# Kernel tuning notes

Measured on AMD Instinct MI355X. Metric: run time of the kernel, lower is better.

## Reference

```python
import jax, jax.numpy as jnp
import numpy as np

N_DIM = 512
HEADS = 8
NUM_EXPERTS = 65536
NUM_KEYS = 256      # sqrt(NUM_EXPERTS)
DIM_KEY = 256       # N_DIM // 2
TOPK = 16           # num_experts_per_head (also product_key_topk)
SCALE = 0.02


def setup_inputs() -> dict:
    key = jax.random.key(0)
    k0, k1, k2, k3, k4 = jax.random.split(key, 5)
    x = jax.random.normal(k0, (1, 2048, N_DIM), dtype=jnp.float32)
    W_q = jax.random.normal(k1, (N_DIM, 2 * HEADS * DIM_KEY), dtype=jnp.float32) * SCALE
    keys = jax.random.normal(k2, (HEADS, NUM_KEYS, 2, DIM_KEY), dtype=jnp.float32) * SCALE
    down_embed = jax.random.normal(k3, (NUM_EXPERTS, N_DIM), dtype=jnp.float32) * SCALE
    up_embed = jax.random.normal(k4, (NUM_EXPERTS, N_DIM), dtype=jnp.float32) * SCALE
    return {"x": x, "W_q": W_q, "keys": keys, "down_embed": down_embed, "up_embed": up_embed}


def reference(x, W_q, keys, down_embed, up_embed):
    b, n, d = x.shape
    # queries: [b,n,2*h*dk] -> [2,b,n,h,dk]
    q = (x @ W_q).reshape(b, n, 2, HEADS, DIM_KEY).transpose(2, 0, 1, 3, 4)
    # similarity against product keys: [2,b,n,h,num_keys]
    sim = jnp.einsum('pbnhd,hkpd->pbnhk', q, keys)
    sx, ix = jax.lax.top_k(sim[0], TOPK)   # [b,n,h,TOPK]
    sy, iy = jax.lax.top_k(sim[1], TOPK)
    # cartesian product of the two top-k sets -> [b,n,h,TOPK*TOPK]
    all_scores = (sx[..., :, None] + sy[..., None, :]).reshape(b, n, HEADS, TOPK * TOPK)
    scores, pk_idx = jax.lax.top_k(all_scores, TOPK)  # [b,n,h,TOPK]
    # NOTE: original module indexes embeddings with pk_idx (flat top-k positions),
    # reproduced faithfully here.
    w_down = down_embed[pk_idx]  # [b,n,h,TOPK,d]
    w_up = up_embed[pk_idx]      # [b,n,h,TOPK,d]
    h = jnp.einsum('bnd,bnhkd->bnhk', x, w_down)
    h = jax.nn.gelu(h, approximate=False)
    h = jax.nn.softmax(scores, axis=-1) * h
    return jnp.einsum('bnhk,bnhkd->bnd', h, w_up)
```

## Files before the change

### kernel.cpp

```cpp
#include <hip/hip_runtime.h>
#include <math.h>

#define N_TOK 2048
#define NDIM 512
#define HEADS 8
#define TOPK 16
#define QCOLS 4096

typedef __attribute__((ext_vector_type(8))) _Float16 f16x8;
typedef __attribute__((ext_vector_type(4))) float f32x4;

__device__ __forceinline__ unsigned short f32_to_f16(float f) {
    _Float16 h = (_Float16)f;
    return __builtin_bit_cast(unsigned short, h);
}
__device__ __forceinline__ float f16_to_f32(unsigned short u) {
    return (float)__builtin_bit_cast(_Float16, u);
}
__device__ __forceinline__ void gl_lds16(const void* g, void* l) {
    __builtin_amdgcn_global_load_lds(
        (const __attribute__((address_space(1))) void*)g,
        (__attribute__((address_space(3))) void*)l, 16, 0, 0);
}

__device__ __forceinline__ void split_f4(const float* __restrict__ src,
                                         unsigned short* __restrict__ dh,
                                         unsigned short* __restrict__ dl,
                                         int i) {
    float4 v = reinterpret_cast<const float4*>(src)[i];
    float vv[4] = {v.x, v.y, v.z, v.w};
    ushort4 h, lo;
    unsigned short* hp = &h.x; unsigned short* lp = &lo.x;
    #pragma unroll
    for (int q = 0; q < 4; ++q) {
        unsigned short hh = f32_to_f16(vv[q]);
        hp[q] = hh;
        lp[q] = f32_to_f16(vv[q] - f16_to_f32(hh));
    }
    reinterpret_cast<ushort4*>(dh)[i] = h;
    reinterpret_cast<ushort4*>(dl)[i] = lo;
}

__global__ __launch_bounds__(256) void kP_split(const float* __restrict__ x,
                                                const float* __restrict__ Wq,
                                                const float* __restrict__ keys,
                                                const float* __restrict__ down,
                                                const float* __restrict__ up,
                                                unsigned short* __restrict__ xh,
                                                unsigned short* __restrict__ xl,
                                                unsigned short* __restrict__ Wqh,
                                                unsigned short* __restrict__ Wql,
                                                unsigned short* __restrict__ ksh,
                                                unsigned short* __restrict__ ksl,
                                                unsigned short* __restrict__ Mth,
                                                unsigned short* __restrict__ Mtl,
                                                unsigned short* __restrict__ upTh,
                                                unsigned short* __restrict__ upTl) {
    const int bid = blockIdx.x;
    const int tid = threadIdx.x;
    if (bid < 256) {
        #pragma unroll
        for (int t = 0; t < 4; ++t) split_f4(x, xh, xl, bid * 1024 + t * 256 + tid);
        return;
    }
    if (bid < 768) {
        const int b = bid - 256;
        #pragma unroll
        for (int t = 0; t < 4; ++t) split_f4(Wq, Wqh, Wql, b * 1024 + t * 256 + tid);
        return;
    }
    if (bid < 1024) {
        const int b = bid - 768;
        #pragma unroll
        for (int t = 0; t < 4; ++t) split_f4(keys, ksh, ksl, b * 1024 + t * 256 + tid);
        return;
    }
    if (bid < 1280) {
        const int e = bid - 1024;
        const int d0 = tid * 2;
        float2 v = *reinterpret_cast<const float2*>(&down[(size_t)e * NDIM + d0]);
        ushort2 h, lo;
        unsigned short h0 = f32_to_f16(v.x);
        unsigned short h1 = f32_to_f16(v.y);
        h.x = h0; h.y = h1;
        lo.x = f32_to_f16(v.x - f16_to_f32(h0));
        lo.y = f32_to_f16(v.y - f16_to_f32(h1));
        *reinterpret_cast<ushort2*>(&Mth[(size_t)(QCOLS + e) * NDIM + d0]) = h;
        *reinterpret_cast<ushort2*>(&Mtl[(size_t)(QCOLS + e) * NDIM + d0]) = lo;
        return;
    }
    const int b = bid - 1280;
    #pragma unroll
    for (int dd = 0; dd < 8; ++dd) {
        const int d = b * 8 + dd;
        const int e = tid;
        const float v = up[(size_t)e * NDIM + d];
        unsigned short hh = f32_to_f16(v);
        upTh[(size_t)d * 256 + e] = hh;
        upTl[(size_t)d * 256 + e] = f32_to_f16(v - f16_to_f32(hh));
    }
}

__global__ __launch_bounds__(256) void kQ_m1(const unsigned short* __restrict__ Wqh,
                                             const unsigned short* __restrict__ Wql,
                                             const unsigned short* __restrict__ ksh,
                                             const unsigned short* __restrict__ ksl,
                                             unsigned short* __restrict__ Mth,
                                             unsigned short* __restrict__ Mtl) {
    __shared__ __align__(16) char lds[36864];
    const int tid = threadIdx.x;
    const int w = tid >> 6, l = tid & 63;
    const int c0 = blockIdx.x * 32;
    const int ph = blockIdx.y;
    const int p = ph >> 3, h = ph & 7;
    const int off = p * 2048 + h * 256;
    f32x4 acc[2][4] = {};

    for (int s = 0; s < 8; ++s) {
        const int kk = s * 32;
        __syncthreads();
        {
            const int q = w * 1024 + l * 16;
            const int r = q >> 7;
            const int bsw = (q & 127) ^ ((r & 7) << 4);
            const unsigned short* src = (bsw < 64)
                ? Wqh + (size_t)(c0 + r) * QCOLS + off + kk + (bsw >> 1)
                : Wql + (size_t)(c0 + r) * QCOLS + off + kk + ((bsw - 64) >> 1);
            gl_lds16(src, lds + w * 1024);
        }
        #pragma unroll
        for (int t = 0; t < 8; ++t) {
            const int q = w * 8192 + t * 1024 + l * 16;
            const int r = q >> 7;
            const int bsw = (q & 127) ^ ((r & 7) << 4);
            const unsigned short* src = (bsw < 64)
                ? ksh + ((size_t)(h * 256 + r) * 2 + p) * 256 + kk + (bsw >> 1)
                : ksl + ((size_t)(h * 256 + r) * 2 + p) * 256 + kk + ((bsw - 64) >> 1);
            gl_lds16(src, lds + 4096 + w * 8192 + t * 1024);
        }
        __syncthreads();
        const int bq = (l >> 4) * 16;
        f16x8 ah[2], al[2];
        #pragma unroll
        for (int mi = 0; mi < 2; ++mi) {
            const int ra = mi * 16 + (l & 15);
            const int swz = (ra & 7) << 4;
            ah[mi] = *(const f16x8*)(lds + ra * 128 + (bq ^ swz));
            al[mi] = *(const f16x8*)(lds + ra * 128 + ((bq + 64) ^ swz));
        }
        __builtin_amdgcn_s_setprio(1);
        #pragma unroll
        for (int nj = 0; nj < 4; ++nj) {
            const int rb = w * 64 + nj * 16 + (l & 15);
            const int swz = (rb & 7) << 4;
            f16x8 bh = *(const f16x8*)(lds + 4096 + rb * 128 + (bq ^ swz));
            f16x8 bl = *(const f16x8*)(lds + 4096 + rb * 128 + ((bq + 64) ^ swz));
            #pragma unroll
            for (int mi = 0; mi < 2; ++mi) {
                acc[mi][nj] = __builtin_amdgcn_mfma_f32_16x16x32_f16(ah[mi], bh, acc[mi][nj], 0, 0, 0);
                acc[mi][nj] = __builtin_amdgcn_mfma_f32_16x16x32_f16(ah[mi], bl, acc[mi][nj], 0, 0, 0);
                acc[mi][nj] = __builtin_amdgcn_mfma_f32_16x16x32_f16(al[mi], bh, acc[mi][nj], 0, 0, 0);
            }
        }
        __builtin_amdgcn_s_setprio(0);
    }
    #pragma unroll
    for (int mi = 0; mi < 2; ++mi)
        #pragma unroll
        for (int nj = 0; nj < 4; ++nj) {
            const int k = w * 64 + nj * 16 + (l & 15);
            const int cb = c0 + mi * 16 + (l >> 4) * 4;
            ushort4 h4, l4;
            unsigned short* hp = &h4.x; unsigned short* lp = &l4.x;
            #pragma unroll
            for (int r = 0; r < 4; ++r) {
                const float v = acc[mi][nj][r];
                unsigned short hh = f32_to_f16(v);
                hp[r] = hh;
                lp[r] = f32_to_f16(v - f16_to_f32(hh));
            }
            *reinterpret_cast<ushort4*>(&Mth[(size_t)(off + k) * NDIM + cb]) = h4;
            *reinterpret_cast<ushort4*>(&Mtl[(size_t)(off + k) * NDIM + cb]) = l4;
        }
}

#define BM 64
#define BN 256
#define BK 32
__global__ __launch_bounds__(256, 3) void kF_gemm(const unsigned short* __restrict__ xh,
                                                  const unsigned short* __restrict__ xl,
                                                  const unsigned short* __restrict__ Mth,
                                                  const unsigned short* __restrict__ Mtl,
                                                  float* __restrict__ T,
                                                  float* __restrict__ D) {
    __shared__ __align__(16) char lds[40960];
    const int tid = threadIdx.x;
    const int w = tid >> 6, l = tid & 63;
    const int row0 = blockIdx.x * BM;
    const int g = blockIdx.y;
    const int colbase = g * 256;
    f32x4 acc[4][4] = {};

    for (int s = 0; s < 16; ++s) {
        const int kk = s * BK;
        __syncthreads();
        #pragma unroll
        for (int t = 0; t < 2; ++t) {
            const int q = w * 2048 + t * 1024 + l * 16;
            const int r = q >> 7;
            const int bsw = (q & 127) ^ ((r & 7) << 4);
            const unsigned short* src = (bsw < 64)
                ? xh + (size_t)(row0 + r) * NDIM + kk + (bsw >> 1)
                : xl + (size_t)(row0 + r) * NDIM + kk + ((bsw - 64) >> 1);
            gl_lds16(src, lds + w * 2048 + t * 1024);
        }
        #pragma unroll
        for (int t = 0; t < 8; ++t) {
            const int q = w * 8192 + t * 1024 + l * 16;
            const int r = q >> 7;
            const int bsw = (q & 127) ^ ((r & 7) << 4);
            const unsigned short* src = (bsw < 64)
                ? Mth + (size_t)(colbase + r) * NDIM + kk + (bsw >> 1)
                : Mtl + (size_t)(colbase + r) * NDIM + kk + ((bsw - 64) >> 1);
            gl_lds16(src, lds + 8192 + w * 8192 + t * 1024);
        }
        __syncthreads();
        const int bq = (l >> 4) * 16;
        f16x8 ah[4], al[4];
        #pragma unroll
        for (int mi = 0; mi < 4; ++mi) {
            const int ra = mi * 16 + (l & 15);
            const int swz = (ra & 7) << 4;
            ah[mi] = *(const f16x8*)(lds + ra * 128 + (bq ^ swz));
            al[mi] = *(const f16x8*)(lds + ra * 128 + ((bq + 64) ^ swz));
        }
        __builtin_amdgcn_s_setprio(1);
        #pragma unroll
        for (int nj = 0; nj < 4; ++nj) {
            const int rb = w * 64 + nj * 16 + (l & 15);
            const int swz = (rb & 7) << 4;
            f16x8 bh = *(const f16x8*)(lds + 8192 + rb * 128 + (bq ^ swz));
            f16x8 bl = *(const f16x8*)(lds + 8192 + rb * 128 + ((bq + 64) ^ swz));
            #pragma unroll
            for (int mi = 0; mi < 4; ++mi) {
                acc[mi][nj] = __builtin_amdgcn_mfma_f32_16x16x32_f16(ah[mi], bh, acc[mi][nj], 0, 0, 0);
                acc[mi][nj] = __builtin_amdgcn_mfma_f32_16x16x32_f16(ah[mi], bl, acc[mi][nj], 0, 0, 0);
                acc[mi][nj] = __builtin_amdgcn_mfma_f32_16x16x32_f16(al[mi], bh, acc[mi][nj], 0, 0, 0);
            }
        }
        __builtin_amdgcn_s_setprio(0);
    }
    __syncthreads();

    if (g == 16) {
        #pragma unroll
        for (int mi = 0; mi < 4; ++mi)
            #pragma unroll
            for (int nj = 0; nj < 4; ++nj)
                #pragma unroll
                for (int r = 0; r < 4; ++r) {
                    const int row = row0 + mi * 16 + (l >> 4) * 4 + r;
                    const int col = w * 64 + nj * 16 + (l & 15);
                    D[(size_t)row * 256 + col] = acc[mi][nj][r];
                }
        return;
    }

    float* Cl = (float*)lds;
    const int grp = tid >> 4;
    const int lam = tid & 15;
    for (int c = 0; c < 4; ++c) {
        #pragma unroll
        for (int nj = 0; nj < 4; ++nj)
            #pragma unroll
            for (int r = 0; r < 4; ++r)
                Cl[((l >> 4) * 4 + r) * 260 + w * 64 + nj * 16 + (l & 15)] = acc[c][nj][r];
        __syncthreads();
        float v[16];
        #pragma unroll
        for (int j = 0; j < 16; ++j) v[j] = Cl[grp * 260 + lam + 16 * j];
        #pragma unroll
        for (int k = 2; k <= 16; k <<= 1)
            #pragma unroll
            for (int j = k >> 1; j > 0; j >>= 1)
                #pragma unroll
                for (int i = 0; i < 16; ++i) {
                    const int l2 = i ^ j;
                    if (l2 > i) {
                        const bool asc = ((i & k) == 0);
                        const float lo = fminf(v[i], v[l2]), hi = fmaxf(v[i], v[l2]);
                        v[i] = asc ? lo : hi;
                        v[l2] = asc ? hi : lo;
                    }
                }
        #pragma unroll
        for (int lvl = 1; lvl <= 8; lvl <<= 1) {
            float m[16];
            #pragma unroll
            for (int q = 0; q < 16; ++q)
                m[q] = fmaxf(v[q], __shfl_xor(v[15 - q], lvl));
            #pragma unroll
            for (int j = 8; j > 0; j >>= 1)
                #pragma unroll
                for (int i = 0; i < 16; ++i) {
                    const int l2 = i ^ j;
                    if (l2 > i) {
                        const float lo = fminf(m[i], m[l2]), hi = fmaxf(m[i], m[l2]);
                        m[i] = lo; m[l2] = hi;
                    }
                }
            #pragma unroll
            for (int q = 0; q < 16; ++q) v[q] = m[q];
        }
        const int n = row0 + c * 16 + grp;
        T[((size_t)n * 16 + g) * 16 + lam] = v[15 - lam];
        __syncthreads();
    }
}

__device__ const unsigned short CAND_TBL[32] = {
    0x0100, 0x0302, 0x0504, 0x0706, 0x0908, 0x0B0A, 0x0D0C, 0x0F0E,
    0x1110, 0x1312, 0x1514, 0x1716,
    0x2120, 0x2322, 0x3024, 0x3231, 0x4033, 0x4241,
    0x5150, 0x6160, 0x7170,
    0x9080, 0xB0A0, 0xD0C0, 0xF0E0,
    0xFFFF, 0xFFFF, 0xFFFF, 0xFFFF, 0xFFFF, 0xFFFF, 0xFFFF
};

__device__ __forceinline__ float sel16(const float a[16], int i) {
    float b0 = (i & 1) ? a[1] : a[0];
    float b1 = (i & 1) ? a[3] : a[2];
    float b2 = (i & 1) ? a[5] : a[4];
    float b3 = (i & 1) ? a[7] : a[6];
    float b4 = (i & 1) ? a[9] : a[8];
    float b5 = (i & 1) ? a[11] : a[10];
    float b6 = (i & 1) ? a[13] : a[12];
    float b7 = (i & 1) ? a[15] : a[14];
    float c0 = (i & 2) ? b1 : b0;
    float c1 = (i & 2) ? b3 : b2;
    float c2 = (i & 2) ? b5 : b4;
    float c3 = (i & 2) ? b7 : b6;
    float d0 = (i & 4) ? c1 : c0;
    float d1 = (i & 4) ? c3 : c2;
    return (i & 8) ? d1 : d0;
}

__global__ __launch_bounds__(256) void kC_combine(const float* __restrict__ T,
                                                  const float* __restrict__ D,
                                                  unsigned short* __restrict__ Wh,
                                                  unsigned short* __restrict__ Wl) {
    __shared__ unsigned long long ckey[8][50];
    __shared__ float winval[8][16];
    __shared__ int winflat[8][16];
    __shared__ int Wrow[256];

    const int tid = threadIdx.x;
    const int n = blockIdx.x;
    const int h = tid >> 5;
    const int lam = tid & 15;

    Wrow[tid] = 0;

    float sxd[16], syd[16];
    const float* t0 = &T[((size_t)n * 16 + h) * 16];
    const float* t1 = &T[((size_t)n * 16 + 8 + h) * 16];
    #pragma unroll
    for (int q = 0; q < 16; ++q) { sxd[q] = t0[q]; syd[q] = t1[q]; }

    const int lc = tid & 31;
    const unsigned int cw = CAND_TBL[lc];
    unsigned long long mykey[2]; float myval[2]; int myflat[2]; int myrank[2] = {0, 0};
    #pragma unroll
    for (int u = 0; u < 2; ++u) {
        const int fl = (cw >> (8 * u)) & 0xFF;
        const float sv = sel16(sxd, fl >> 4) + sel16(syd, fl & 15);
        const unsigned int uv = __float_as_uint(sv);
        const unsigned int mo = (uv & 0x80000000u) ? ~uv : (uv | 0x80000000u);
        mykey[u] = ((unsigned long long)mo << 8) | (unsigned long long)(255 - fl);
        myval[u] = sv; myflat[u] = fl;
        const int slot = lc * 2 + u;
        if (slot < 50) ckey[h][slot] = mykey[u];
    }
    __syncthreads();
    for (int kk = 0; kk < 50; ++kk) {
        const unsigned long long ok = ckey[h][kk];
        myrank[0] += (ok > mykey[0]) ? 1 : 0;
        myrank[1] += (ok > mykey[1]) ? 1 : 0;
    }
    #pragma unroll
    for (int u = 0; u < 2; ++u)
        if (myrank[u] < 16) { winval[h][myrank[u]] = myval[u]; winflat[h][myrank[u]] = myflat[u]; }
    __syncthreads();

    if (!(tid & 16)) {
        const float sc = winval[h][lam];
        const float m0 = winval[h][0];
        float e = expf(sc - m0);
        float esum = e;
        #pragma unroll
        for (int off = 1; off < 16; off <<= 1) esum += __shfl_xor(esum, off);
        const int fl = winflat[h][lam];
        const float hv = D[(size_t)n * 256 + fl];
        const float gg = 0.5f * hv * (1.0f + erff(hv * 0.70710678118654752f));
        const float wv = (e / esum) * gg;
        atomicAdd(&Wrow[fl], __float2int_rn(wv * 4194304.0f));
    }
    __syncthreads();
    const float wfin = (float)Wrow[tid] * (1.0f / 4194304.0f);
    const unsigned short hh = f32_to_f16(wfin);
    Wh[(size_t)n * 256 + tid] = hh;
    Wl[(size_t)n * 256 + tid] = f32_to_f16(wfin - f16_to_f32(hh));
}

__global__ __launch_bounds__(256) void k5_mfma(const unsigned short* __restrict__ Wh,
                                               const unsigned short* __restrict__ Wl,
                                               const unsigned short* __restrict__ upTh,
                                               const unsigned short* __restrict__ upTl,
                                               float* __restrict__ out) {
    __shared__ __align__(16) char lds[20480];
    const int tid = threadIdx.x;
    const int w = tid >> 6, l = tid & 63;
    const int n0 = blockIdx.x * 32;
    const int d0 = blockIdx.y * 128;
    f32x4 acc[2][2] = {};

    for (int s = 0; s < 8; ++s) {
        const int kk = s * 32;
        __syncthreads();
        {
            const int q = w * 1024 + l * 16;
            const int r = q >> 7;
            const int bsw = (q & 127) ^ ((r & 7) << 4);
            const unsigned short* src = (bsw < 64)
                ? Wh + (size_t)(n0 + r) * 256 + kk + (bsw >> 1)
                : Wl + (size_t)(n0 + r) * 256 + kk + ((bsw - 64) >> 1);
            gl_lds16(src, lds + w * 1024);
        }
        #pragma unroll
        for (int t = 0; t < 4; ++t) {
            const int q = w * 4096 + t * 1024 + l * 16;
            const int r = q >> 7;
            const int bsw = (q & 127) ^ ((r & 7) << 4);
            const unsigned short* src = (bsw < 64)
                ? upTh + (size_t)(d0 + r) * 256 + kk + (bsw >> 1)
                : upTl + (size_t)(d0 + r) * 256 + kk + ((bsw - 64) >> 1);
            gl_lds16(src, lds + 4096 + w * 4096 + t * 1024);
        }
        __syncthreads();
        const int bq = (l >> 4) * 16;
        f16x8 ah[2], al[2];
        #pragma unroll
        for (int mi = 0; mi < 2; ++mi) {
            const int ra = mi * 16 + (l & 15);
            const int swz = (ra & 7) << 4;
            ah[mi] = *(const f16x8*)(lds + ra * 128 + (bq ^ swz));
            al[mi] = *(const f16x8*)(lds + ra * 128 + ((bq + 64) ^ swz));
        }
        #pragma unroll
        for (int nj = 0; nj < 2; ++nj) {
            const int rb = w * 32 + nj * 16 + (l & 15);
            const int swz = (rb & 7) << 4;
            f16x8 bh = *(const f16x8*)(lds + 4096 + rb * 128 + (bq ^ swz));
            f16x8 bl = *(const f16x8*)(lds + 4096 + rb * 128 + ((bq + 64) ^ swz));
            #pragma unroll
            for (int mi = 0; mi < 2; ++mi) {
                acc[mi][nj] = __builtin_amdgcn_mfma_f32_16x16x32_f16(ah[mi], bh, acc[mi][nj], 0, 0, 0);
                acc[mi][nj] = __builtin_amdgcn_mfma_f32_16x16x32_f16(ah[mi], bl, acc[mi][nj], 0, 0, 0);
                acc[mi][nj] = __builtin_amdgcn_mfma_f32_16x16x32_f16(al[mi], bh, acc[mi][nj], 0, 0, 0);
            }
        }
    }
    #pragma unroll
    for (int mi = 0; mi < 2; ++mi)
        #pragma unroll
        for (int nj = 0; nj < 2; ++nj)
            #pragma unroll
            for (int r = 0; r < 4; ++r) {
                const int row = n0 + mi * 16 + (l >> 4) * 4 + r;
                const int col = d0 + w * 32 + nj * 16 + (l & 15);
                out[(size_t)row * NDIM + col] = acc[mi][nj][r];
            }
}

extern "C" void kernel_launch(void* const* d_in, const int* in_sizes, int n_in,
                              void* d_out, int out_size, void* d_ws, size_t ws_size,
                              hipStream_t stream) {
    const float* x    = (const float*)d_in[0];
    const float* Wq   = (const float*)d_in[1];
    const float* keys = (const float*)d_in[2];
    const float* down = (const float*)d_in[3];
    const float* up   = (const float*)d_in[4];
    float* out = (float*)d_out;

    char* ws = (char*)d_ws;
    unsigned short* Mth  = (unsigned short*)(ws);
    unsigned short* Mtl  = (unsigned short*)(ws + 4456448);
    unsigned short* xh   = (unsigned short*)(ws + 8912896);
    unsigned short* xl   = (unsigned short*)(ws + 11010048);
    unsigned short* Wqh  = (unsigned short*)(ws + 13107200);
    unsigned short* Wql  = (unsigned short*)(ws + 17301504);
    unsigned short* ksh  = (unsigned short*)(ws + 21495808);
    unsigned short* ksl  = (unsigned short*)(ws + 23592960);
    unsigned short* upTh = (unsigned short*)(ws + 25690112);
    unsigned short* upTl = (unsigned short*)(ws + 25952256);
    float* T             = (float*)(ws + 26214400);
    float* D             = (float*)(ws + 28311552);
    unsigned short* Wh   = (unsigned short*)(ws + 30408704);
    unsigned short* Wl   = (unsigned short*)(ws + 31457280);

    kP_split<<<1344, 256, 0, stream>>>(x, Wq, keys, down, up,
                                       xh, xl, Wqh, Wql, ksh, ksl, Mth, Mtl, upTh, upTl);
    kQ_m1<<<dim3(16, 16), 256, 0, stream>>>(Wqh, Wql, ksh, ksl, Mth, Mtl);
    kF_gemm<<<dim3(32, 17), 256, 0, stream>>>(xh, xl, Mth, Mtl, T, D);
    kC_combine<<<2048, 256, 0, stream>>>(T, D, Wh, Wl);
    k5_mfma<<<dim3(64, 4), 256, 0, stream>>>(Wh, Wl, upTh, upTl, out);
}
```

Before: 94.20 us.

## Retile score GEMM to 128x128 with double-buffered LDS and split top-k merge

The fused score GEMM moves from 64x256 tiles to 128x128 tiles and double-buffers the LDS stages, so the next K-slice loads while MFMAs run. Each block now produces top-16 over 128 keys instead of 256, which doubles the partial-list layout in T. The combine kernel gains a bitonic merge of two 16-element partial lists per half-key. The intent is better load/compute overlap and a grid shape that fills the CUs better, at the cost of lower occupancy (launch bounds 2), more T traffic and extra merge work in the combine kernel.

Measured after the change: 91.51 us. -2.8%, faster.

```diff
diff --git a/kernel.cpp b/kernel.cpp
--- a/kernel.cpp
+++ b/kernel.cpp
@@ -184,101 +184,112 @@
         }
 }
 
-#define BM 64
-#define BN 256
+#define BM 128
+#define BN 128
 #define BK 32
-__global__ __launch_bounds__(256, 3) void kF_gemm(const unsigned short* __restrict__ xh,
+#define KFBUF 32768
+__global__ __launch_bounds__(256, 2) void kF_gemm(const unsigned short* __restrict__ xh,
                                                   const unsigned short* __restrict__ xl,
                                                   const unsigned short* __restrict__ Mth,
                                                   const unsigned short* __restrict__ Mtl,
                                                   float* __restrict__ T,
                                                   float* __restrict__ D) {
-    __shared__ __align__(16) char lds[40960];
+    __shared__ __align__(16) char lds[2 * KFBUF];
     const int tid = threadIdx.x;
     const int w = tid >> 6, l = tid & 63;
     const int row0 = blockIdx.x * BM;
-    const int g = blockIdx.y;
-    const int colbase = g * 256;
-    f32x4 acc[4][4] = {};
-
-    for (int s = 0; s < 16; ++s) {
+    const int by = blockIdx.y;
+    const int colbase = by * 128;
+    f32x4 acc[8][2] = {};
+
+    auto stage = [&](int buf, int s) {
         const int kk = s * BK;
-        __syncthreads();
-        #pragma unroll
-        for (int t = 0; t < 2; ++t) {
-            const int q = w * 2048 + t * 1024 + l * 16;
+        char* base = lds + buf * KFBUF;
+        #pragma unroll
+        for (int t = 0; t < 4; ++t) {
+            const int q = w * 4096 + t * 1024 + l * 16;
             const int r = q >> 7;
             const int bsw = (q & 127) ^ ((r & 7) << 4);
             const unsigned short* src = (bsw < 64)
                 ? xh + (size_t)(row0 + r) * NDIM + kk + (bsw >> 1)
                 : xl + (size_t)(row0 + r) * NDIM + kk + ((bsw - 64) >> 1);
-            gl_lds16(src, lds + w * 2048 + t * 1024);
-        }
-        #pragma unroll
-        for (int t = 0; t < 8; ++t) {
-            const int q = w * 8192 + t * 1024 + l * 16;
+            gl_lds16(src, base + w * 4096 + t * 1024);
+        }
+        #pragma unroll
+        for (int t = 0; t < 4; ++t) {
+            const int q = w * 4096 + t * 1024 + l * 16;
             const int r = q >> 7;
             const int bsw = (q & 127) ^ ((r & 7) << 4);
             const unsigned short* src = (bsw < 64)
                 ? Mth + (size_t)(colbase + r) * NDIM + kk + (bsw >> 1)
                 : Mtl + (size_t)(colbase + r) * NDIM + kk + ((bsw - 64) >> 1);
-            gl_lds16(src, lds + 8192 + w * 8192 + t * 1024);
-        }
-        __syncthreads();
+            gl_lds16(src, base + 16384 + w * 4096 + t * 1024);
+        }
+    };
+
+    stage(0, 0);
+    __syncthreads();
+    for (int s = 0; s < 16; ++s) {
+        if (s + 1 < 16) stage((s + 1) & 1, s + 1);
+        const char* base = lds + (s & 1) * KFBUF;
         const int bq = (l >> 4) * 16;
-        f16x8 ah[4], al[4];
-        #pragma unroll
-        for (int mi = 0; mi < 4; ++mi) {
+        f16x8 bh[2], bl[2];
+        #pragma unroll
+        for (int nj = 0; nj < 2; ++nj) {
+            const int rb = w * 32 + nj * 16 + (l & 15);
+            const int swz = (rb & 7) << 4;
+            bh[nj] = *(const f16x8*)(base + 16384 + rb * 128 + (bq ^ swz));
+            bl[nj] = *(const f16x8*)(base + 16384 + rb * 128 + ((bq + 64) ^ swz));
+        }
+        __builtin_amdgcn_s_setprio(1);
+        #pragma unroll
+        for (int mi = 0; mi < 8; ++mi) {
             const int ra = mi * 16 + (l & 15);
             const int swz = (ra & 7) << 4;
-            ah[mi] = *(const f16x8*)(lds + ra * 128 + (bq ^ swz));
-            al[mi] = *(const f16x8*)(lds + ra * 128 + ((bq + 64) ^ swz));
-        }
-        __builtin_amdgcn_s_setprio(1);
-        #pragma unroll
-        for (int nj = 0; nj < 4; ++nj) {
-            const int rb = w * 64 + nj * 16 + (l & 15);
-            const int swz = (rb & 7) << 4;
-            f16x8 bh = *(const f16x8*)(lds + 8192 + rb * 128 + (bq ^ swz));
-            f16x8 bl = *(const f16x8*)(lds + 8192 + rb * 128 + ((bq + 64) ^ swz));
-            #pragma unroll
-            for (int mi = 0; mi < 4; ++mi) {
-                acc[mi][nj] = __builtin_amdgcn_mfma_f32_16x16x32_f16(ah[mi], bh, acc[mi][nj], 0, 0, 0);
-                acc[mi][nj] = __builtin_amdgcn_mfma_f32_16x16x32_f16(ah[mi], bl, acc[mi][nj], 0, 0, 0);
-                acc[mi][nj] = __builtin_amdgcn_mfma_f32_16x16x32_f16(al[mi], bh, acc[mi][nj], 0, 0, 0);
+            f16x8 ah = *(const f16x8*)(base + ra * 128 + (bq ^ swz));
+            f16x8 al = *(const f16x8*)(base + ra * 128 + ((bq + 64) ^ swz));
+            #pragma unroll
+            for (int nj = 0; nj < 2; ++nj) {
+                acc[mi][nj] = __builtin_amdgcn_mfma_f32_16x16x32_f16(ah, bh[nj], acc[mi][nj], 0, 0, 0);
+                acc[mi][nj] = __builtin_amdgcn_mfma_f32_16x16x32_f16(ah, bl[nj], acc[mi][nj], 0, 0, 0);
+                acc[mi][nj] = __builtin_amdgcn_mfma_f32_16x16x32_f16(al, bh[nj], acc[mi][nj], 0, 0, 0);
             }
         }
         __builtin_amdgcn_s_setprio(0);
-    }
-    __syncthreads();
-
-    if (g == 16) {
-        #pragma unroll
-        for (int mi = 0; mi < 4; ++mi)
-            #pragma unroll
-            for (int nj = 0; nj < 4; ++nj)
+        __syncthreads();
+    }
+
+    if (by >= 32) {
+        #pragma unroll
+        for (int mi = 0; mi < 8; ++mi)
+            #pragma unroll
+            for (int nj = 0; nj < 2; ++nj)
                 #pragma unroll
                 for (int r = 0; r < 4; ++r) {
                     const int row = row0 + mi * 16 + (l >> 4) * 4 + r;
-                    const int col = w * 64 + nj * 16 + (l & 15);
+                    const int col = (by - 32) * 128 + w * 32 + nj * 16 + (l & 15);
                     D[(size_t)row * 256 + col] = acc[mi][nj][r];
                 }
         return;
     }
 
     float* Cl = (float*)lds;
-    const int grp = tid >> 4;
-    const int lam = tid & 15;
+    const int grp8 = tid >> 3;
+    const int lam8 = tid & 7;
     for (int c = 0; c < 4; ++c) {
         #pragma unroll
-        for (int nj = 0; nj < 4; ++nj)
-            #pragma unroll
-            for (int r = 0; r < 4; ++r)
-                Cl[((l >> 4) * 4 + r) * 260 + w * 64 + nj * 16 + (l & 15)] = acc[c][nj][r];
+        for (int mm = 0; mm < 2; ++mm) {
+            const int mi = c * 2 + mm;
+            #pragma unroll
+            for (int nj = 0; nj < 2; ++nj)
+                #pragma unroll
+                for (int r = 0; r < 4; ++r)
+                    Cl[(mm * 16 + (l >> 4) * 4 + r) * 136 + w * 32 + nj * 16 + (l & 15)] = acc[mi][nj][r];
+        }
         __syncthreads();
         float v[16];
         #pragma unroll
-        for (int j = 0; j < 16; ++j) v[j] = Cl[grp * 260 + lam + 16 * j];
+        for (int j = 0; j < 16; ++j) v[j] = Cl[grp8 * 136 + lam8 + 8 * j];
         #pragma unroll
         for (int k = 2; k <= 16; k <<= 1)
             #pragma unroll
@@ -294,7 +305,7 @@
                     }
                 }
         #pragma unroll
-        for (int lvl = 1; lvl <= 8; lvl <<= 1) {
+        for (int lvl = 1; lvl <= 4; lvl <<= 1) {
             float m[16];
             #pragma unroll
             for (int q = 0; q < 16; ++q)
@@ -312,8 +323,9 @@
             #pragma unroll
             for (int q = 0; q < 16; ++q) v[q] = m[q];
         }
-        const int n = row0 + c * 16 + grp;
-        T[((size_t)n * 16 + g) * 16 + lam] = v[15 - lam];
+        const int n = row0 + c * 32 + grp8;
+        T[((size_t)n * 32 + by) * 16 + 2 * lam8]     = v[15 - 2 * lam8];
+        T[((size_t)n * 32 + by) * 16 + 2 * lam8 + 1] = v[14 - 2 * lam8];
         __syncthreads();
     }
 }
@@ -345,6 +357,30 @@
     return (i & 8) ? d1 : d0;
 }
 
+__device__ __forceinline__ void merge_desc16(const float* __restrict__ a,
+                                             const float* __restrict__ b,
+                                             float out_desc[16]) {
+    float m[16];
+    #pragma unroll
+    for (int q = 0; q < 16; ++q) m[q] = fmaxf(a[q], b[15 - q]);
+    #pragma unroll
+    for (int k = 2; k <= 16; k <<= 1)
+        #pragma unroll
+        for (int j = k >> 1; j > 0; j >>= 1)
+            #pragma unroll
+            for (int i = 0; i < 16; ++i) {
+                const int l2 = i ^ j;
+                if (l2 > i) {
+                    const bool asc = ((i & k) == 0);
+                    const float lo = fminf(m[i], m[l2]), hi = fmaxf(m[i], m[l2]);
+                    m[i] = asc ? lo : hi;
+                    m[l2] = asc ? hi : lo;
+                }
+            }
+    #pragma unroll
+    for (int q = 0; q < 16; ++q) out_desc[q] = m[15 - q];
+}
+
 __global__ __launch_bounds__(256) void kC_combine(const float* __restrict__ T,
                                                   const float* __restrict__ D,
                                                   unsigned short* __restrict__ Wh,
@@ -361,11 +397,19 @@
 
     Wrow[tid] = 0;
 
+    float a0[16], a1[16], b0v[16], b1v[16];
+    const float* t00 = &T[((size_t)n * 32 + 2 * h) * 16];
+    const float* t01 = &T[((size_t)n * 32 + 2 * h + 1) * 16];
+    const float* t10 = &T[((size_t)n * 32 + 16 + 2 * h) * 16];
+    const float* t11 = &T[((size_t)n * 32 + 17 + 2 * h) * 16];
+    #pragma unroll
+    for (int q = 0; q < 16; ++q) {
+        a0[q] = t00[q]; a1[q] = t01[q];
+        b0v[q] = t10[q]; b1v[q] = t11[q];
+    }
     float sxd[16], syd[16];
-    const float* t0 = &T[((size_t)n * 16 + h) * 16];
-    const float* t1 = &T[((size_t)n * 16 + 8 + h) * 16];
-    #pragma unroll
-    for (int q = 0; q < 16; ++q) { sxd[q] = t0[q]; syd[q] = t1[q]; }
+    merge_desc16(a0, a1, sxd);
+    merge_desc16(b0v, b1v, syd);
 
     const int lc = tid & 31;
     const unsigned int cw = CAND_TBL[lc];
@@ -504,14 +548,14 @@
     unsigned short* upTh = (unsigned short*)(ws + 25690112);
     unsigned short* upTl = (unsigned short*)(ws + 25952256);
     float* T             = (float*)(ws + 26214400);
-    float* D             = (float*)(ws + 28311552);
-    unsigned short* Wh   = (unsigned short*)(ws + 30408704);
-    unsigned short* Wl   = (unsigned short*)(ws + 31457280);
+    float* D             = (float*)(ws + 30408704);
+    unsigned short* Wh   = (unsigned short*)(ws + 32505856);
+    unsigned short* Wl   = (unsigned short*)(ws + 33554432);
 
     kP_split<<<1344, 256, 0, stream>>>(x, Wq, keys, down, up,
                                        xh, xl, Wqh, Wql, ksh, ksl, Mth, Mtl, upTh, upTl);
     kQ_m1<<<dim3(16, 16), 256, 0, stream>>>(Wqh, Wql, ksh, ksl, Mth, Mtl);
-    kF_gemm<<<dim3(32, 17), 256, 0, stream>>>(xh, xl, Mth, Mtl, T, D);
+    kF_gemm<<<dim3(16, 34), 256, 0, stream>>>(xh, xl, Mth, Mtl, T, D);
     kC_combine<<<2048, 256, 0, stream>>>(T, D, Wh, Wl);
     k5_mfma<<<dim3(64, 4), 256, 0, stream>>>(Wh, Wl, upTh, upTl, out);
 }
```
